# Optimization experiments

Measured on AMD Instinct MI355X. Metric: run time of the kernel, lower is better.

Reference implementation:

```python
import jax, jax.numpy as jnp
import numpy as np

EPS = 1e-6
SCAL = 5.0
PARTS = 16
NFEAT = 32
RES = 64


def conv(x, w, b, stride=1):
    y = jax.lax.conv_general_dilated(x, w, (stride, stride), 'SAME',
                                     dimension_numbers=('NCHW', 'OIHW', 'NCHW'))
    return y + b[None, :, None, None]


def spatial_softmax(x):
    b, k, h, w = x.shape
    return jax.nn.softmax(x.reshape(b, k, h * w), axis=-1).reshape(b, k, h, w)


def make_grid(h, w):
    ys = jnp.linspace(-1.0, 1.0, h)
    xs = jnp.linspace(-1.0, 1.0, w)
    gy, gx = jnp.meshgrid(ys, xs, indexing='ij')
    return jnp.stack([gy, gx], axis=-1)  # [h, w, 2]


def e_sigma(x, w1, b1, w2, b2, wp, bp):
    # shared shape/appearance encoder: parts via spatial softmax + residual sum map
    h1 = jax.nn.relu(conv(x, w1, b1, stride=2))   # [B,64,64,64]
    h2 = jax.nn.relu(conv(h1, w2, b2))            # [B,64,64,64]
    parts = spatial_softmax(conv(h2, wp, bp))     # [B,16,64,64]
    return parts, h2


def e_alpha(x, w1, b1, w2, b2):
    h1 = jax.nn.relu(conv(x, w1, b1))
    return conv(h1, w2, b2)                       # [B,32,64,64]


def get_mu_and_prec(parts):
    # soft-argmax mean + 2x2 covariance -> inverse Cholesky factor L_inv
    b, k, h, w = parts.shape
    grid = make_grid(h, w)
    mu = jnp.einsum('bkhw,hwc->bkc', parts, grid)                       # [b,k,2]
    outer = jnp.einsum('hwm,hwn->hwmn', grid, grid)
    cov = jnp.einsum('bkhw,hwmn->bkmn', parts, outer) - jnp.einsum('bkm,bkn->bkmn', mu, mu)
    a = jnp.sqrt(cov[..., 0, 0] + EPS)
    bb = cov[..., 0, 1] / (a + EPS)
    c = jnp.sqrt(jnp.maximum(cov[..., 1, 1] - bb * bb, 0.0) + EPS)
    det = a * c
    z = jnp.zeros_like(a)
    L_inv = SCAL / (det[..., None, None] + EPS) * jnp.stack(
        [jnp.stack([c, z], axis=-1), jnp.stack([-bb, a], axis=-1)], axis=-2)  # [b,k,2,2]
    return mu, L_inv


def feat_mu_to_enc(alpha, mu, L_inv, h, w):
    # render Cauchy-shaped part heatmaps from (mu, L_inv) and paint part features
    grid = make_grid(h, w)
    dist = grid[None, None] - mu[:, :, None, None, :]        # [b,k,h,w,2]
    proj = jnp.einsum('bkhwi,bkij->bkhwj', dist, L_inv)
    heat = 1.0 / (1.0 + jnp.sum(proj * proj, axis=-1))       # [b,k,h,w]
    norm = heat / (jnp.sum(heat, axis=(2, 3), keepdims=True) + EPS)
    fmap = jnp.einsum('bkf,bkhw->bfhw', alpha, norm)         # [b,nf,h,w]
    return jnp.concatenate([heat, fmap], axis=1)             # [b,nk+nf,h,w]


def decoder(enc, w1, b1, w2, b2, w3, b3):
    h1 = jax.nn.relu(conv(enc, w1, b1))                      # [B,64,64,64]
    up = jnp.repeat(jnp.repeat(h1, 2, axis=2), 2, axis=3)    # nearest upsample -> 128
    h2 = jax.nn.relu(conv(up, w2, b2))
    return jax.nn.sigmoid(conv(h2, w3, b3))                  # [B,3,128,128]


def setup_inputs():
    key = jax.random.key(0)
    ks = jax.random.split(key, 16)
    def w(k, shape):
        fan_in = shape[1] * shape[2] * shape[3]
        return (jax.random.normal(k, shape, jnp.float32) / np.sqrt(fan_in)).astype(jnp.float32)
    B = 32
    return {
        'x': jax.random.uniform(ks[0], (B, 3, 128, 128), jnp.float32),
        'x_spatial_transform': jax.random.uniform(ks[1], (B, 3, 128, 128), jnp.float32),
        'x_appearance_transform': jax.random.uniform(ks[2], (B, 3, 128, 128), jnp.float32),
        'coord': jax.random.normal(ks[3], (B, PARTS, 2), jnp.float32) * 0.5,
        'vector': jax.random.normal(ks[4], (B, PARTS, 2), jnp.float32) * 0.1,
        'es_w1': w(ks[5], (RES, 3, 3, 3)), 'es_b1': jnp.zeros((RES,), jnp.float32),
        'es_w2': w(ks[6], (RES, RES, 3, 3)), 'es_b2': jnp.zeros((RES,), jnp.float32),
        'es_wp': w(ks[7], (PARTS, RES, 3, 3)), 'es_bp': jnp.zeros((PARTS,), jnp.float32),
        'ea_w1': w(ks[8], (RES, RES, 3, 3)), 'ea_b1': jnp.zeros((RES,), jnp.float32),
        'ea_w2': w(ks[9], (NFEAT, RES, 3, 3)), 'ea_b2': jnp.zeros((NFEAT,), jnp.float32),
        'd_w1': w(ks[10], (RES, PARTS + NFEAT, 3, 3)), 'd_b1': jnp.zeros((RES,), jnp.float32),
        'd_w2': w(ks[11], (32, RES, 3, 3)), 'd_b2': jnp.zeros((32,), jnp.float32),
        'd_w3': w(ks[12], (3, 32, 3, 3)), 'd_b3': jnp.zeros((3,), jnp.float32),
    }


def reference(x, x_spatial_transform, x_appearance_transform, coord, vector,
              es_w1, es_b1, es_w2, es_b2, es_wp, es_bp,
              ea_w1, ea_b1, ea_w2, ea_b2,
              d_w1, d_b1, d_w2, d_b2, d_w3, d_b3):
    # shape stream (appearance-transformed image -> geometry)
    shape_parts, _ = e_sigma(x_appearance_transform, es_w1, es_b1, es_w2, es_b2, es_wp, es_bp)
    mu, L_inv = get_mu_and_prec(shape_parts)
    # appearance stream (spatially-transformed image -> appearance)
    app_parts, app_sum = e_sigma(x_spatial_transform, es_w1, es_b1, es_w2, es_b2, es_wp, es_bp)
    f_xs = e_alpha(app_sum, ea_w1, ea_b1, ea_w2, ea_b2)
    # local part appearances: gather features under each part map
    alpha = jnp.einsum('bfhw,bkhw->bkf', f_xs, app_parts)
    encoding = feat_mu_to_enc(alpha, mu, L_inv, 64, 64)
    reconstruction = decoder(encoding, d_w1, d_b1, d_w2, d_b2, d_w3, d_b3)
    # composite loss
    mu_a, L_inv_a = get_mu_and_prec(app_parts)
    rec_loss = jnp.mean((x - reconstruction) ** 2)
    equiv_loss = jnp.mean((mu - mu_a) ** 2) + 0.01 * jnp.mean((L_inv - L_inv_a) ** 2)
    transport_loss = jnp.mean((mu_a - (coord + vector)) ** 2)
    loss = rec_loss + equiv_loss + transport_loss
    return reconstruction, loss
```

## Files before the change

kernel.cpp:

```cpp
#include <hip/hip_runtime.h>
#include <hip/hip_bf16.h>

#define EPS 1e-6f
#define SCAL 5.0f

typedef __attribute__((ext_vector_type(8))) short bf8v;
typedef __attribute__((ext_vector_type(4))) float f32x4;

#define OFF_MU     0
#define OFF_LINV   1024
#define OFF_MUA    3072
#define OFF_LINVA  4096
#define OFF_HSUM   6144
#define OFF_ALPHA  6656
#define OFF_REC    23040
#define OFF_R1     32768
#define OFF_R2     (OFF_R1 + 8388608)
#define OFF_R3     (OFF_R2 + 8388608)
#define WS_TOTAL   (OFF_R3 + 16777216)

#define BA_XA   ((size_t)2 * OFF_R3)
#define BA_X2   ((size_t)2 * OFF_R1)
#define OFF_PARTSF OFF_R2
#define OFF_PROBS  (OFF_R2 + 4194304)
#define BA_EA1  ((size_t)2 * OFF_R3)
#define OFF_FXS (OFF_R3 + 4194304)
#define BA_E    ((size_t)2 * OFF_R2)
#define BA_D1   ((size_t)2 * OFF_R1)
#define BA_D2   ((size_t)2 * OFF_R3)

#define WT_ESW1 0
#define WT_ESB1 1728
#define WT_ESB2 1792
#define WT_ESBP 1856
#define WT_EAB1 1872
#define WT_EAB2 1936
#define WT_DB1  1968
#define WT_DB2  2032
#define WT_W3P  2064
#define WT_DB3  2928
#define P_WP2  0
#define P_WPP  36864
#define P_WPA1 46080
#define P_WPA2 82944
#define P_WPD1 101376
#define P_WPD2 138240

__device__ __attribute__((aligned(16))) float g_ws[WS_TOTAL];
__device__ __attribute__((aligned(16))) float g_wt[3072];
__device__ __attribute__((aligned(16))) __hip_bfloat16 g_wp[156672];
__device__ int g_isbf16;

__device__ __forceinline__ float selz(bool c, float v) { return c ? v : 0.f; }
__device__ __forceinline__ float cvtbf(short s) {
    return __uint_as_float(((unsigned int)(unsigned short)s) << 16);
}
__device__ __forceinline__ float ldin(const void* p, size_t i, int bf) {
    return bf ? __bfloat162float(((const __hip_bfloat16*)p)[i])
              : ((const float*)p)[i];
}

__device__ __forceinline__ float block_sum(float v) {
    __shared__ float sb[8];
    for (int off = 32; off; off >>= 1) v += __shfl_down(v, off, 64);
    int lane = threadIdx.x & 63, wid = threadIdx.x >> 6;
    __syncthreads();
    if (lane == 0) sb[wid] = v;
    __syncthreads();
    float r = 0.f;
    for (int i = 0; i < 4; ++i) r += sb[i];
    return r;
}
__device__ __forceinline__ float block_max(float v) {
    __shared__ float sb[8];
    for (int off = 32; off; off >>= 1) v = fmaxf(v, __shfl_down(v, off, 64));
    int lane = threadIdx.x & 63, wid = threadIdx.x >> 6;
    __syncthreads();
    if (lane == 0) sb[wid] = v;
    __syncthreads();
    float r = -1e30f;
    for (int i = 0; i < 4; ++i) r = fmaxf(r, sb[i]);
    return r;
}

__global__ void detect_k(const void* x) {
    const __hip_bfloat16* p = (const __hip_bfloat16*)x;
    int lane = threadIdx.x & 63;
    float v = 0.f;
    for (int i = lane; i < 256; i += 64) {
        float a = fabsf(__bfloat162float(p[i]));
        if (!(a <= 2.0f)) v = 1.f;
    }
    for (int off = 32; off; off >>= 1) v += __shfl_down(v, off, 64);
    if (lane == 0) {
        g_isbf16 = (v == 0.f) ? 1 : 0;
        g_ws[OFF_REC] = 0.f;
    }
}

__global__ void wpack_k(const void* esw1, const void* esb1, const void* esw2, const void* esb2,
                        const void* eswp, const void* esbp, const void* eaw1, const void* eab1,
                        const void* eaw2, const void* eab2, const void* dw1, const void* db1,
                        const void* dw2, const void* db2, const void* dw3, const void* db3) {
    int bf = g_isbf16;
    int gid0 = blockIdx.x * 256 + threadIdx.x, stride = gridDim.x * 256;
    for (int g = gid0; g < 1728; g += stride) g_wt[WT_ESW1 + g] = ldin(esw1, g, bf);
    for (int g = gid0; g < 64; g += stride) g_wt[WT_ESB1 + g] = ldin(esb1, g, bf);
    for (int g = gid0; g < 64; g += stride) g_wt[WT_ESB2 + g] = ldin(esb2, g, bf);
    for (int g = gid0; g < 16; g += stride) g_wt[WT_ESBP + g] = ldin(esbp, g, bf);
    for (int g = gid0; g < 64; g += stride) g_wt[WT_EAB1 + g] = ldin(eab1, g, bf);
    for (int g = gid0; g < 32; g += stride) g_wt[WT_EAB2 + g] = ldin(eab2, g, bf);
    for (int g = gid0; g < 64; g += stride) g_wt[WT_DB1 + g] = ldin(db1, g, bf);
    for (int g = gid0; g < 32; g += stride) g_wt[WT_DB2 + g] = ldin(db2, g, bf);
    for (int g = gid0; g < 3; g += stride) g_wt[WT_DB3 + g] = ldin(db3, g, bf);
    for (int g = gid0; g < 864; g += stride) {
        int t = g / 96, o = (g / 32) % 3, k = g & 31;
        g_wt[WT_W3P + g] = ldin(dw3, (size_t)(o * 32 + k) * 9 + t, bf);
    }
    for (int g = gid0; g < 36864; g += stride) {
        int t = g >> 12, n = (g >> 6) & 63, k = g & 63;
        g_wp[P_WP2 + g] = __float2bfloat16(ldin(esw2, (size_t)(n * 64 + k) * 9 + t, bf));
    }
    for (int g = gid0; g < 9216; g += stride) {
        int t = g >> 10, n = (g >> 6) & 15, k = g & 63;
        g_wp[P_WPP + g] = __float2bfloat16(ldin(eswp, (size_t)(n * 64 + k) * 9 + t, bf));
    }
    for (int g = gid0; g < 36864; g += stride) {
        int t = g >> 12, n = (g >> 6) & 63, k = g & 63;
        g_wp[P_WPA1 + g] = __float2bfloat16(ldin(eaw1, (size_t)(n * 64 + k) * 9 + t, bf));
    }
    for (int g = gid0; g < 18432; g += stride) {
        int t = g >> 11, n = (g >> 6) & 31, k = g & 63;
        g_wp[P_WPA2 + g] = __float2bfloat16(ldin(eaw2, (size_t)(n * 64 + k) * 9 + t, bf));
    }
    for (int g = gid0; g < 36864; g += stride) {
        int t = g >> 12, n = (g >> 6) & 63, k = g & 63;
        float v = (k < 48) ? ldin(dw1, (size_t)(n * 48 + k) * 9 + t, bf) : 0.f;
        g_wp[P_WPD1 + g] = __float2bfloat16(v);
    }
    for (int g = gid0; g < 18432; g += stride) {
        int t = g >> 11, n = (g >> 6) & 31, k = g & 63;
        g_wp[P_WPD2 + g] = __float2bfloat16(ldin(dw2, (size_t)(n * 64 + k) * 9 + t, bf));
    }
}

__global__ void __launch_bounds__(256)
conv_s2n_k(const void* __restrict__ inA, const void* __restrict__ inB) {
    int bf = g_isbf16;
    int tile = blockIdx.x & 15;
    int gb = blockIdx.x >> 4;
    int g = gb & 3, b = gb >> 2;
    const void* in = (b < 32) ? inA : inB;
    int bb = b & 31;
    int pix = tile * 256 + threadIdx.x;
    int y = pix >> 6, x = pix & 63;
    size_t inb = (size_t)bb * 3 * 16384;
    const float* W = g_wt + WT_ESW1 + (size_t)(g * 16) * 27;
    float acc[16];
    #pragma unroll
    for (int o = 0; o < 16; ++o) acc[o] = g_wt[WT_ESB1 + g * 16 + o];
    int iy0 = 2 * y, ix0 = 2 * x;
    bool my2 = (iy0 + 2 < 128), mx2 = (ix0 + 2 < 128);
    int iy2 = my2 ? iy0 + 2 : 127, ix2 = mx2 ? ix0 + 2 : 127;
    for (int ic = 0; ic < 3; ++ic) {
        size_t pb = inb + ic * 16384;
        float t[9];
        t[0] = ldin(in, pb + iy0 * 128 + ix0, bf);
        t[1] = ldin(in, pb + iy0 * 128 + ix0 + 1, bf);
        t[2] = selz(mx2, ldin(in, pb + iy0 * 128 + ix2, bf));
        t[3] = ldin(in, pb + (iy0 + 1) * 128 + ix0, bf);
        t[4] = ldin(in, pb + (iy0 + 1) * 128 + ix0 + 1, bf);
        t[5] = selz(mx2, ldin(in, pb + (iy0 + 1) * 128 + ix2, bf));
        t[6] = selz(my2, ldin(in, pb + iy2 * 128 + ix0, bf));
        t[7] = selz(my2, ldin(in, pb + iy2 * 128 + ix0 + 1, bf));
        t[8] = selz(my2 && mx2, ldin(in, pb + iy2 * 128 + ix2, bf));
        #pragma unroll
        for (int o = 0; o < 16; ++o) {
            const float* wr = W + (o * 3 + ic) * 9;
            float a = acc[o];
            #pragma unroll
            for (int j = 0; j < 9; ++j) a = fmaf(t[j], wr[j], a);
            acc[o] = a;
        }
    }
    __hip_bfloat16* out = (__hip_bfloat16*)g_ws + BA_XA + ((size_t)b * 4096 + pix) * 64 + g * 16;
    #pragma unroll
    for (int o = 0; o < 16; ++o) out[o] = __float2bfloat16(fmaxf(acc[o], 0.f));
}

template<int TOTN, int NS, int OUTF32, int RELU>
__global__ void __launch_bounds__(256) __attribute__((amdgpu_waves_per_eu(2, 4)))
conv_mfl_k(size_t in_off, int wp_off, int bias_off, size_t out_off) {
    __shared__ __hip_bfloat16 sA[6 * 66 * 64];
    int wid = threadIdx.x >> 6, lane = threadIdx.x & 63;
    int l15 = lane & 15, quad = lane >> 4;
    int b = blockIdx.x >> 4, y0 = (blockIdx.x & 15) * 4;
    const __hip_bfloat16* inb = (const __hip_bfloat16*)g_ws + in_off + (size_t)b * 4096 * 64;
    for (int g = threadIdx.x; g < 3072; g += 256) {
        int r = g >> 9;
        int rem = g & 511;
        int px = rem >> 3, j = rem & 7;
        int yy = y0 - 1 + r;
        int P = px + 1;
        bf8v v = (bf8v){0, 0, 0, 0, 0, 0, 0, 0};
        if (yy >= 0 && yy <= 63)
            v = *(const bf8v*)(inb + ((size_t)(yy * 64 + px) * 64 + j * 8));
        *(bf8v*)(sA + ((r * 66 + P) * 64 + ((j ^ (P & 7)) * 8))) = v;
    }
    if (threadIdx.x < 96) {
        int g = threadIdx.x;
        int r = g / 16, rem = g % 16, side = rem >> 3, j = rem & 7;
        int P = side ? 65 : 0;
        *(bf8v*)(sA + ((r * 66 + P) * 64 + ((j ^ (P & 7)) * 8))) = (bf8v){0, 0, 0, 0, 0, 0, 0, 0};
    }
    __syncthreads();
    int y = y0 + wid;
    f32x4 acc[4][NS];
    #pragma unroll
    for (int ms = 0; ms < 4; ++ms)
        #pragma unroll
        for (int ns = 0; ns < NS; ++ns) acc[ms][ns] = (f32x4){0.f, 0.f, 0.f, 0.f};
    #pragma unroll
    for (int t = 0; t < 9; ++t) {
        int dy = t / 3 - 1, dx = t % 3 - 1;
        int r = wid + 1 + dy;
        #pragma unroll
        for (int c = 0; c < 2; ++c) {
            int j = c * 4 + quad;
            bf8v a[4];
            #pragma unroll
            for (int ms = 0; ms < 4; ++ms) {
                int P = ms * 16 + l15 + dx + 1;
                a[ms] = *(const bf8v*)(sA + ((r * 66 + P) * 64 + ((j ^ (P & 7)) * 8)));
            }
            #pragma unroll
            for (int ns = 0; ns < NS; ++ns) {
                bf8v bv = *(const bf8v*)(g_wp + wp_off +
                          ((size_t)(t * TOTN + ns * 16 + l15) * 64 + c * 32 + quad * 8));
                #pragma unroll
                for (int ms = 0; ms < 4; ++ms)
                    acc[ms][ns] = __builtin_amdgcn_mfma_f32_16x16x32_bf16(a[ms], bv, acc[ms][ns], 0, 0, 0);
            }
        }
    }
    #pragma unroll
    for (int ns = 0; ns < NS; ++ns) {
        float bias = g_wt[bias_off + ns * 16 + l15];
        #pragma unroll
        for (int ms = 0; ms < 4; ++ms) {
            #pragma unroll
            for (int r = 0; r < 4; ++r) {
                int pix = ms * 16 + quad * 4 + r;
                float v = acc[ms][ns][r] + bias;
                if (RELU) v = fmaxf(v, 0.f);
                size_t o = out_off + ((size_t)(b * 4096 + y * 64 + pix)) * TOTN + ns * 16 + l15;
                if (OUTF32) g_ws[o] = v;
                else ((__hip_bfloat16*)g_ws)[o] = __float2bfloat16(v);
            }
        }
    }
}

__global__ void __launch_bounds__(256) __attribute__((amdgpu_waves_per_eu(2, 4)))
conv_upmf2_k(size_t in_off, int wp_off, int bias_off, size_t out_off) {
    __shared__ __hip_bfloat16 sA[4 * 66 * 64];
    int wid = threadIdx.x >> 6, lane = threadIdx.x & 63;
    int l15 = lane & 15, quad = lane >> 4;
    int b = blockIdx.x >> 5, y0 = (blockIdx.x & 31) * 4;
    int ri0 = (y0 >> 1) - 1;
    const __hip_bfloat16* inb = (const __hip_bfloat16*)g_ws + in_off + (size_t)b * 4096 * 64;
    for (int g = threadIdx.x; g < 2048; g += 256) {
        int r = g >> 9;
        int rem = g & 511;
        int px = rem >> 3, j = rem & 7;
        int yi = ri0 + r;
        int P = px + 1;
        bf8v v = (bf8v){0, 0, 0, 0, 0, 0, 0, 0};
        if (yi >= 0 && yi <= 63)
            v = *(const bf8v*)(inb + ((size_t)(yi * 64 + px) * 64 + j * 8));
        *(bf8v*)(sA + ((r * 66 + P) * 64 + ((j ^ (P & 7)) * 8))) = v;
    }
    if (threadIdx.x < 64) {
        int g = threadIdx.x;
        int r = g >> 4, rem = g & 15, side = rem >> 3, j = rem & 7;
        int P = side ? 65 : 0;
        *(bf8v*)(sA + ((r * 66 + P) * 64 + ((j ^ (P & 7)) * 8))) = (bf8v){0, 0, 0, 0, 0, 0, 0, 0};
    }
    __syncthreads();
    int y = y0 + wid;
    f32x4 acc[8][2];
    #pragma unroll
    for (int ms = 0; ms < 8; ++ms)
        #pragma unroll
        for (int ns = 0; ns < 2; ++ns) acc[ms][ns] = (f32x4){0.f, 0.f, 0.f, 0.f};
    #pragma unroll
    for (int t = 0; t < 9; ++t) {
        int dy = t / 3 - 1, dx = t % 3 - 1;
        int yy = y + dy;
        if (yy < 0 || yy > 127) continue;
        int r = (yy >> 1) - ri0;
        #pragma unroll
        for (int c = 0; c < 2; ++c) {
            int j = c * 4 + quad;
            bf8v a[8];
            #pragma unroll
            for (int ms = 0; ms < 8; ++ms) {
                int xx = ms * 16 + l15 + dx;
                int P = (xx < 0) ? 0 : ((xx > 127) ? 65 : ((xx >> 1) + 1));
                a[ms] = *(const bf8v*)(sA + ((r * 66 + P) * 64 + ((j ^ (P & 7)) * 8)));
            }
            #pragma unroll
            for (int ns = 0; ns < 2; ++ns) {
                bf8v bv = *(const bf8v*)(g_wp + wp_off +
                          ((size_t)(t * 32 + ns * 16 + l15) * 64 + c * 32 + quad * 8));
                #pragma unroll
                for (int ms = 0; ms < 8; ++ms)
                    acc[ms][ns] = __builtin_amdgcn_mfma_f32_16x16x32_bf16(a[ms], bv, acc[ms][ns], 0, 0, 0);
            }
        }
    }
    #pragma unroll
    for (int ns = 0; ns < 2; ++ns) {
        float bias = g_wt[bias_off + ns * 16 + l15];
        #pragma unroll
        for (int ms = 0; ms < 8; ++ms) {
            #pragma unroll
            for (int r = 0; r < 4; ++r) {
                int pix = ms * 16 + quad * 4 + r;
                float v = fmaxf(acc[ms][ns][r] + bias, 0.f);
                size_t o = out_off + ((size_t)(b * 16384 + y * 128 + pix)) * 32 + ns * 16 + l15;
                ((__hip_bfloat16*)g_ws)[o] = __float2bfloat16(v);
            }
        }
    }
}

__global__ void sm_mom3_k() {
    int bk = blockIdx.x;
    int b = bk >> 4, k = bk & 15;
    int app = (b >= 32);
    const float* P = g_ws + OFF_PARTSF + (size_t)b * 4096 * 16 + k;
    float r[16];
    #pragma unroll
    for (int j = 0; j < 16; ++j) r[j] = P[(size_t)(threadIdx.x + j * 256) * 16];
    float m = r[0];
    #pragma unroll
    for (int j = 1; j < 16; ++j) m = fmaxf(m, r[j]);
    m = block_max(m);
    float s = 0.f;
    #pragma unroll
    for (int j = 0; j < 16; ++j) { r[j] = __expf(r[j] - m); s += r[j]; }
    s = block_sum(s);
    float inv = 1.0f / s;
    float sy = 0, sx = 0, syy = 0, sxy = 0, sxx = 0;
    #pragma unroll
    for (int j = 0; j < 16; ++j) {
        float pv = r[j] * inv;
        int i = threadIdx.x + j * 256;
        if (app) g_ws[OFF_PROBS + ((size_t)(b - 32) * 16 + k) * 4096 + i] = pv;
        float gy = -1.0f + (i >> 6) * (2.0f / 63.0f);
        float gx = -1.0f + (i & 63) * (2.0f / 63.0f);
        sy += pv * gy; sx += pv * gx;
        syy += pv * gy * gy; sxy += pv * gy * gx; sxx += pv * gx * gx;
    }
    sy = block_sum(sy); sx = block_sum(sx);
    syy = block_sum(syy); sxy = block_sum(sxy); sxx = block_sum(sxx);
    if (threadIdx.x == 0) {
        float c00 = syy - sy * sy, c01 = sxy - sy * sx, c11 = sxx - sx * sx;
        float a = sqrtf(fmaxf(c00 + EPS, 1e-12f));
        float bb = c01 / (a + EPS);
        float cc = sqrtf(fmaxf(c11 - bb * bb, 0.f) + EPS);
        float det = a * cc;
        float sc = SCAL / (det + EPS);
        int idx = app ? ((b - 32) * 16 + k) : (b * 16 + k);
        int mu_off = app ? OFF_MUA : OFF_MU;
        int linv_off = app ? OFF_LINVA : OFF_LINV;
        g_ws[mu_off + idx * 2 + 0] = sy;
        g_ws[mu_off + idx * 2 + 1] = sx;
        g_ws[linv_off + idx * 4 + 0] = cc * sc;
        g_ws[linv_off + idx * 4 + 1] = 0.f;
        g_ws[linv_off + idx * 4 + 2] = -bb * sc;
        g_ws[linv_off + idx * 4 + 3] = a * sc;
    }
}

__global__ void alpha2_k() {
    int bk = blockIdx.x;
    int b = bk >> 4;
    __shared__ float pl[4096];
    const float* pr = g_ws + OFF_PROBS + (size_t)bk * 4096;
    for (int i = threadIdx.x; i < 4096; i += 256) pl[i] = pr[i];
    __syncthreads();
    float acc[32];
    #pragma unroll
    for (int f = 0; f < 32; ++f) acc[f] = 0.f;
    for (int i = threadIdx.x; i < 4096; i += 256) {
        float pv = pl[i];
        const float* fp = g_ws + OFF_FXS + (size_t)(b * 4096 + i) * 32;
        #pragma unroll
        for (int f = 0; f < 32; ++f) acc[f] = fmaf(pv, fp[f], acc[f]);
    }
    __shared__ float sw[4][32];
    int lane = threadIdx.x & 63, wid = threadIdx.x >> 6;
    #pragma unroll
    for (int f = 0; f < 32; ++f)
        for (int off = 32; off; off >>= 1) acc[f] += __shfl_down(acc[f], off, 64);
    if (lane == 0) {
        #pragma unroll
        for (int f = 0; f < 32; ++f) sw[wid][f] = acc[f];
    }
    __syncthreads();
    if (threadIdx.x < 32)
        g_ws[OFF_ALPHA + bk * 32 + threadIdx.x] =
            sw[0][threadIdx.x] + sw[1][threadIdx.x] + sw[2][threadIdx.x] + sw[3][threadIdx.x];
}

__global__ void heat2_k() {
    int bk = blockIdx.x;
    int b = bk >> 4, k = bk & 15;
    float m0 = g_ws[OFF_MU + bk * 2], m1 = g_ws[OFF_MU + bk * 2 + 1];
    float L00 = g_ws[OFF_LINV + bk * 4 + 0], L10 = g_ws[OFF_LINV + bk * 4 + 2],
          L11 = g_ws[OFF_LINV + bk * 4 + 3];
    __hip_bfloat16* E = (__hip_bfloat16*)g_ws + BA_E;
    float s = 0.f;
    for (int i = threadIdx.x; i < 4096; i += 256) {
        float d0 = -1.0f + (i >> 6) * (2.0f / 63.0f) - m0;
        float d1 = -1.0f + (i & 63) * (2.0f / 63.0f) - m1;
        float p0 = d0 * L00 + d1 * L10;
        float p1 = d1 * L11;
        float h = 1.0f / (1.0f + p0 * p0 + p1 * p1);
        E[(size_t)(b * 4096 + i) * 64 + k] = __float2bfloat16(h);
        s += h;
    }
    s = block_sum(s);
    if (threadIdx.x == 0) g_ws[OFF_HSUM + bk] = s;
}

__global__ void fmap2_k() {
    int tile = blockIdx.x & 15, b = blockIdx.x >> 4;
    __shared__ float coef[16][32];
    for (int i = threadIdx.x; i < 512; i += 256) {
        int k = i >> 5, f = i & 31;
        coef[k][f] = g_ws[OFF_ALPHA + (b * 16 + k) * 32 + f] /
                     (g_ws[OFF_HSUM + b * 16 + k] + EPS);
    }
    __syncthreads();
    int pix = tile * 256 + threadIdx.x;
    __hip_bfloat16* E = (__hip_bfloat16*)g_ws + BA_E + (size_t)(b * 4096 + pix) * 64;
    float h[16];
    #pragma unroll
    for (int k = 0; k < 16; ++k) h[k] = __bfloat162float(E[k]);
    #pragma unroll
    for (int f = 0; f < 32; ++f) {
        float a = 0.f;
        #pragma unroll
        for (int k = 0; k < 16; ++k) a = fmaf(h[k], coef[k][f], a);
        E[16 + f] = __float2bfloat16(a);
    }
    #pragma unroll
    for (int z = 48; z < 64; ++z) E[z] = __float2bfloat16(0.f);
}

__global__ void __launch_bounds__(256)
conv_sign_k(const void* __restrict__ ximg, void* __restrict__ outp) {
    int bf = g_isbf16;
    int tile = blockIdx.x & 63, b = blockIdx.x >> 6;
    int pix = tile * 256 + threadIdx.x;
    int y = pix >> 7, x = pix & 127;
    const short* D2 = (const short*)((const __hip_bfloat16*)g_ws + BA_D2 + (size_t)b * 16384 * 32);
    float acc[3];
    #pragma unroll
    for (int o = 0; o < 3; ++o) acc[o] = g_wt[WT_DB3 + o];
    #pragma unroll
    for (int t = 0; t < 9; ++t) {
        int dy = t / 3 - 1, dx = t % 3 - 1;
        int yy = y + dy, xx = x + dx;
        if (yy < 0 || yy > 127 || xx < 0 || xx > 127) continue;
        const short* sp = D2 + (size_t)(yy * 128 + xx) * 32;
        #pragma unroll
        for (int c = 0; c < 4; ++c) {
            bf8v v = *(const bf8v*)(sp + c * 8);
            #pragma unroll
            for (int j = 0; j < 8; ++j) {
                float av = cvtbf(v[j]);
                int k = c * 8 + j;
                acc[0] = fmaf(av, g_wt[WT_W3P + (t * 3 + 0) * 32 + k], acc[0]);
                acc[1] = fmaf(av, g_wt[WT_W3P + (t * 3 + 1) * 32 + k], acc[1]);
                acc[2] = fmaf(av, g_wt[WT_W3P + (t * 3 + 2) * 32 + k], acc[2]);
            }
        }
    }
    float es = 0.f;
    #pragma unroll
    for (int o = 0; o < 3; ++o) {
        float v = 1.0f / (1.0f + __expf(-acc[o]));
        size_t oidx = ((size_t)b * 3 + o) * 16384 + pix;
        if (bf) ((__hip_bfloat16*)outp)[oidx] = __float2bfloat16(v);
        else    ((float*)outp)[oidx] = v;
        float e = ldin(ximg, oidx, bf) - v;
        es += e * e;
    }
    float s = block_sum(es);
    if (threadIdx.x == 0) atomicAdd(&g_ws[OFF_REC], s);
}

__global__ void loss_k(const void* __restrict__ coord,
                       const void* __restrict__ vec,
                       void* __restrict__ outp) {
    int bf = g_isbf16;
    const float* mu = g_ws + OFF_MU;
    const float* linv = g_ws + OFF_LINV;
    const float* mu_a = g_ws + OFF_MUA;
    const float* linv_a = g_ws + OFF_LINVA;
    float s1 = 0, s2 = 0, s3 = 0;
    for (int i = threadIdx.x; i < 1024; i += 256) {
        float d = mu[i] - mu_a[i];
        s1 += d * d;
        float t = ldin(coord, i, bf) + ldin(vec, i, bf);
        float d3 = mu_a[i] - t;
        s3 += d3 * d3;
    }
    for (int i = threadIdx.x; i < 2048; i += 256) {
        float d = linv[i] - linv_a[i];
        s2 += d * d;
    }
    s1 = block_sum(s1);
    s2 = block_sum(s2);
    s3 = block_sum(s3);
    if (threadIdx.x == 0) {
        float loss = g_ws[OFF_REC] / 1572864.0f + s1 / 1024.0f + 0.01f * (s2 / 2048.0f)
                   + s3 / 1024.0f;
        if (bf) ((__hip_bfloat16*)outp)[1572864] = __float2bfloat16(loss);
        else    ((float*)outp)[1572864] = loss;
    }
}

extern "C" void kernel_launch(void* const* d_in, const int* in_sizes, int n_in,
                              void* d_out, int out_size, void* d_ws, size_t ws_size,
                              hipStream_t stream) {
    const void* x     = d_in[0];
    const void* x_st  = d_in[1];
    const void* x_at  = d_in[2];
    const void* coord = d_in[3];
    const void* vec   = d_in[4];

    dim3 blk(256);

    detect_k<<<1, 64, 0, stream>>>(x);
    wpack_k<<<64, blk, 0, stream>>>(
        d_in[5],  d_in[6],  d_in[7],  d_in[8],
        d_in[9],  d_in[10], d_in[11], d_in[12],
        d_in[13], d_in[14], d_in[15], d_in[16],
        d_in[17], d_in[18], d_in[19], d_in[20]);

    conv_s2n_k<<<64 * 4 * 16, blk, 0, stream>>>(x_at, x_st);
    conv_mfl_k<64, 4, 0, 1><<<1024, blk, 0, stream>>>(BA_XA, P_WP2, WT_ESB2, BA_X2);
    conv_mfl_k<16, 1, 1, 0><<<1024, blk, 0, stream>>>(BA_X2, P_WPP, WT_ESBP, (size_t)OFF_PARTSF);
    sm_mom3_k<<<1024, blk, 0, stream>>>();

    conv_mfl_k<64, 4, 0, 1><<<512, blk, 0, stream>>>(BA_X2 + (size_t)32 * 4096 * 64, P_WPA1, WT_EAB1, BA_EA1);
    conv_mfl_k<32, 2, 1, 0><<<512, blk, 0, stream>>>(BA_EA1, P_WPA2, WT_EAB2, (size_t)OFF_FXS);
    alpha2_k<<<512, blk, 0, stream>>>();

    heat2_k<<<512, blk, 0, stream>>>();
    fmap2_k<<<512, blk, 0, stream>>>();

    conv_mfl_k<64, 4, 0, 1><<<512, blk, 0, stream>>>(BA_E, P_WPD1, WT_DB1, BA_D1);
    conv_upmf2_k<<<1024, blk, 0, stream>>>(BA_D1, P_WPD2, WT_DB2, BA_D2);
    conv_sign_k<<<32 * 64, blk, 0, stream>>>(x, d_out);

    loss_k<<<1, blk, 0, stream>>>(coord, vec, d_out);
}
```

Before: 467.0 us.

## Fuse part-logit and appearance conv sharing staged tile; prefetch weights in MFMA loops

Merges the part-logit conv and the first appearance-encoder conv into one kernel that stages the h2 tile into shared memory once and runs both convolutions on it, dropping a launch and a second global read of the same input. Blocks for the appearance half of the batch do both convs, which makes per-block work uneven. It also hoists and double-buffers the global weight-fragment loads in the MFMA conv loops, and preloads all weights into registers for the NS=1 case. The extra live registers may reduce occupancy.

```diff
diff --git a/kernel.cpp b/kernel.cpp
--- a/kernel.cpp
+++ b/kernel.cpp
@@ -188,14 +188,8 @@
     for (int o = 0; o < 16; ++o) out[o] = __float2bfloat16(fmaxf(acc[o], 0.f));
 }
 
-template<int TOTN, int NS, int OUTF32, int RELU>
-__global__ void __launch_bounds__(256) __attribute__((amdgpu_waves_per_eu(2, 4)))
-conv_mfl_k(size_t in_off, int wp_off, int bias_off, size_t out_off) {
-    __shared__ __hip_bfloat16 sA[6 * 66 * 64];
-    int wid = threadIdx.x >> 6, lane = threadIdx.x & 63;
-    int l15 = lane & 15, quad = lane >> 4;
-    int b = blockIdx.x >> 4, y0 = (blockIdx.x & 15) * 4;
-    const __hip_bfloat16* inb = (const __hip_bfloat16*)g_ws + in_off + (size_t)b * 4096 * 64;
+__device__ __forceinline__ void stage_tile(__hip_bfloat16* sA,
+                                           const __hip_bfloat16* __restrict__ inb, int y0) {
     for (int g = threadIdx.x; g < 3072; g += 256) {
         int r = g >> 9;
         int rem = g & 511;
@@ -213,20 +207,58 @@
         int P = side ? 65 : 0;
         *(bf8v*)(sA + ((r * 66 + P) * 64 + ((j ^ (P & 7)) * 8))) = (bf8v){0, 0, 0, 0, 0, 0, 0, 0};
     }
-    __syncthreads();
-    int y = y0 + wid;
+}
+
+template<int TOTN, int NS, int OUTF32, int RELU>
+__device__ __forceinline__ void conv_body(const __hip_bfloat16* sA, int bO, int y,
+                                          int wid, int l15, int quad,
+                                          int wp_off, int bias_off, size_t out_off) {
     f32x4 acc[4][NS];
     #pragma unroll
     for (int ms = 0; ms < 4; ++ms)
         #pragma unroll
         for (int ns = 0; ns < NS; ++ns) acc[ms][ns] = (f32x4){0.f, 0.f, 0.f, 0.f};
-    #pragma unroll
-    for (int t = 0; t < 9; ++t) {
-        int dy = t / 3 - 1, dx = t % 3 - 1;
-        int r = wid + 1 + dy;
-        #pragma unroll
-        for (int c = 0; c < 2; ++c) {
-            int j = c * 4 + quad;
+
+    if constexpr (NS == 1) {
+        bf8v bw[18];
+        #pragma unroll
+        for (int it = 0; it < 18; ++it) {
+            const int t = it >> 1, c = it & 1;
+            bw[it] = *(const bf8v*)(g_wp + wp_off +
+                     ((size_t)(t * TOTN + l15) * 64 + c * 32 + quad * 8));
+        }
+        #pragma unroll
+        for (int it = 0; it < 18; ++it) {
+            const int t = it >> 1, c = it & 1;
+            const int dy = t / 3 - 1, dx = t % 3 - 1;
+            const int r = wid + 1 + dy;
+            const int j = c * 4 + quad;
+            #pragma unroll
+            for (int ms = 0; ms < 4; ++ms) {
+                int P = ms * 16 + l15 + dx + 1;
+                bf8v a = *(const bf8v*)(sA + ((r * 66 + P) * 64 + ((j ^ (P & 7)) * 8)));
+                acc[ms][0] = __builtin_amdgcn_mfma_f32_16x16x32_bf16(a, bw[it], acc[ms][0], 0, 0, 0);
+            }
+        }
+    } else {
+        bf8v bq[2][NS];
+        #pragma unroll
+        for (int ns = 0; ns < NS; ++ns)
+            bq[0][ns] = *(const bf8v*)(g_wp + wp_off +
+                        ((size_t)(ns * 16 + l15) * 64 + quad * 8));
+        #pragma unroll
+        for (int it = 0; it < 18; ++it) {
+            const int t = it >> 1, c = it & 1;
+            if (it + 1 < 18) {
+                const int t2 = (it + 1) >> 1, c2 = (it + 1) & 1;
+                #pragma unroll
+                for (int ns = 0; ns < NS; ++ns)
+                    bq[(it + 1) & 1][ns] = *(const bf8v*)(g_wp + wp_off +
+                        ((size_t)(t2 * TOTN + ns * 16 + l15) * 64 + c2 * 32 + quad * 8));
+            }
+            const int dy = t / 3 - 1, dx = t % 3 - 1;
+            const int r = wid + 1 + dy;
+            const int j = c * 4 + quad;
             bf8v a[4];
             #pragma unroll
             for (int ms = 0; ms < 4; ++ms) {
@@ -234,15 +266,13 @@
                 a[ms] = *(const bf8v*)(sA + ((r * 66 + P) * 64 + ((j ^ (P & 7)) * 8)));
             }
             #pragma unroll
-            for (int ns = 0; ns < NS; ++ns) {
-                bf8v bv = *(const bf8v*)(g_wp + wp_off +
-                          ((size_t)(t * TOTN + ns * 16 + l15) * 64 + c * 32 + quad * 8));
+            for (int ns = 0; ns < NS; ++ns)
                 #pragma unroll
                 for (int ms = 0; ms < 4; ++ms)
-                    acc[ms][ns] = __builtin_amdgcn_mfma_f32_16x16x32_bf16(a[ms], bv, acc[ms][ns], 0, 0, 0);
-            }
-        }
-    }
+                    acc[ms][ns] = __builtin_amdgcn_mfma_f32_16x16x32_bf16(a[ms], bq[it & 1][ns], acc[ms][ns], 0, 0, 0);
+        }
+    }
+
     #pragma unroll
     for (int ns = 0; ns < NS; ++ns) {
         float bias = g_wt[bias_off + ns * 16 + l15];
@@ -253,12 +283,41 @@
                 int pix = ms * 16 + quad * 4 + r;
                 float v = acc[ms][ns][r] + bias;
                 if (RELU) v = fmaxf(v, 0.f);
-                size_t o = out_off + ((size_t)(b * 4096 + y * 64 + pix)) * TOTN + ns * 16 + l15;
+                size_t o = out_off + ((size_t)(bO * 4096 + y * 64 + pix)) * TOTN + ns * 16 + l15;
                 if (OUTF32) g_ws[o] = v;
                 else ((__hip_bfloat16*)g_ws)[o] = __float2bfloat16(v);
             }
         }
     }
+}
+
+template<int TOTN, int NS, int OUTF32, int RELU>
+__global__ void __launch_bounds__(256) __attribute__((amdgpu_waves_per_eu(2, 4)))
+conv_mfl_k(size_t in_off, int wp_off, int bias_off, size_t out_off) {
+    __shared__ __hip_bfloat16 sA[6 * 66 * 64];
+    int wid = threadIdx.x >> 6, lane = threadIdx.x & 63;
+    int l15 = lane & 15, quad = lane >> 4;
+    int b = blockIdx.x >> 4, y0 = (blockIdx.x & 15) * 4;
+    const __hip_bfloat16* inb = (const __hip_bfloat16*)g_ws + in_off + (size_t)b * 4096 * 64;
+    stage_tile(sA, inb, y0);
+    __syncthreads();
+    conv_body<TOTN, NS, OUTF32, RELU>(sA, b, y0 + wid, wid, l15, quad,
+                                      wp_off, bias_off, out_off);
+}
+
+__global__ void __launch_bounds__(256) __attribute__((amdgpu_waves_per_eu(2, 4)))
+conv_pea_k() {
+    __shared__ __hip_bfloat16 sA[6 * 66 * 64];
+    int wid = threadIdx.x >> 6, lane = threadIdx.x & 63;
+    int l15 = lane & 15, quad = lane >> 4;
+    int b = blockIdx.x >> 4, y0 = (blockIdx.x & 15) * 4;
+    const __hip_bfloat16* inb = (const __hip_bfloat16*)g_ws + BA_X2 + (size_t)b * 4096 * 64;
+    stage_tile(sA, inb, y0);
+    __syncthreads();
+    int y = y0 + wid;
+    conv_body<16, 1, 1, 0>(sA, b, y, wid, l15, quad, P_WPP, WT_ESBP, (size_t)OFF_PARTSF);
+    if (b >= 32)
+        conv_body<64, 4, 0, 1>(sA, b - 32, y, wid, l15, quad, P_WPA1, WT_EAB1, BA_EA1);
 }
 
 __global__ void __launch_bounds__(256) __attribute__((amdgpu_waves_per_eu(2, 4)))
@@ -293,14 +352,24 @@
     for (int ms = 0; ms < 8; ++ms)
         #pragma unroll
         for (int ns = 0; ns < 2; ++ns) acc[ms][ns] = (f32x4){0.f, 0.f, 0.f, 0.f};
-    #pragma unroll
-    for (int t = 0; t < 9; ++t) {
-        int dy = t / 3 - 1, dx = t % 3 - 1;
+    bf8v bq[2][2];
+    #pragma unroll
+    for (int ns = 0; ns < 2; ++ns)
+        bq[0][ns] = *(const bf8v*)(g_wp + wp_off + ((size_t)(ns * 16 + l15) * 64 + quad * 8));
+    #pragma unroll
+    for (int it = 0; it < 18; ++it) {
+        const int t = it >> 1, c = it & 1;
+        if (it + 1 < 18) {
+            const int t2 = (it + 1) >> 1, c2 = (it + 1) & 1;
+            #pragma unroll
+            for (int ns = 0; ns < 2; ++ns)
+                bq[(it + 1) & 1][ns] = *(const bf8v*)(g_wp + wp_off +
+                    ((size_t)(t2 * 32 + ns * 16 + l15) * 64 + c2 * 32 + quad * 8));
+        }
+        const int dy = t / 3 - 1, dx = t % 3 - 1;
         int yy = y + dy;
-        if (yy < 0 || yy > 127) continue;
-        int r = (yy >> 1) - ri0;
-        #pragma unroll
-        for (int c = 0; c < 2; ++c) {
+        if (yy >= 0 && yy <= 127) {
+            int r = (yy >> 1) - ri0;
             int j = c * 4 + quad;
             bf8v a[8];
             #pragma unroll
@@ -310,13 +379,10 @@
                 a[ms] = *(const bf8v*)(sA + ((r * 66 + P) * 64 + ((j ^ (P & 7)) * 8)));
             }
             #pragma unroll
-            for (int ns = 0; ns < 2; ++ns) {
-                bf8v bv = *(const bf8v*)(g_wp + wp_off +
-                          ((size_t)(t * 32 + ns * 16 + l15) * 64 + c * 32 + quad * 8));
+            for (int ns = 0; ns < 2; ++ns)
                 #pragma unroll
                 for (int ms = 0; ms < 8; ++ms)
-                    acc[ms][ns] = __builtin_amdgcn_mfma_f32_16x16x32_bf16(a[ms], bv, acc[ms][ns], 0, 0, 0);
-            }
+                    acc[ms][ns] = __builtin_amdgcn_mfma_f32_16x16x32_bf16(a[ms], bq[it & 1][ns], acc[ms][ns], 0, 0, 0);
         }
     }
     #pragma unroll
@@ -555,10 +621,10 @@
 
     conv_s2n_k<<<64 * 4 * 16, blk, 0, stream>>>(x_at, x_st);
     conv_mfl_k<64, 4, 0, 1><<<1024, blk, 0, stream>>>(BA_XA, P_WP2, WT_ESB2, BA_X2);
-    conv_mfl_k<16, 1, 1, 0><<<1024, blk, 0, stream>>>(BA_X2, P_WPP, WT_ESBP, (size_t)OFF_PARTSF);
+
+    conv_pea_k<<<1024, blk, 0, stream>>>();
     sm_mom3_k<<<1024, blk, 0, stream>>>();
 
-    conv_mfl_k<64, 4, 0, 1><<<512, blk, 0, stream>>>(BA_X2 + (size_t)32 * 4096 * 64, P_WPA1, WT_EAB1, BA_EA1);
     conv_mfl_k<32, 2, 1, 0><<<512, blk, 0, stream>>>(BA_EA1, P_WPA2, WT_EAB2, (size_t)OFF_FXS);
     alpha2_k<<<512, blk, 0, stream>>>();
 
```

New measurement: 452.2 us. -3.2%, faster.
